# Kernel tuning notes

Measured on AMD Instinct MI355X. Metric: run time of the kernel, lower is better.

## Reference

```python
import jax, jax.numpy as jnp
import numpy as np

D_MODEL = 1024
HEADS = 16
D_K = D_MODEL // HEADS
D_FF = 4096
EPS = 1e-6


def setup_inputs() -> dict:
    key = jax.random.key(0)
    ks = jax.random.split(key, 20)
    B, S, D = 8, 1024, D_MODEL
    sc = 1.0 / np.sqrt(D)
    scf = 1.0 / np.sqrt(D_FF)
    inp = {
        "x": jax.random.normal(ks[0], (B, S, D), jnp.float32),
        "mask": jnp.ones((B, 1, 1, S), jnp.int32),
        "wq": jax.random.normal(ks[1], (D, D), jnp.float32) * sc,
        "bq": jnp.zeros((D,), jnp.float32),
        "wk": jax.random.normal(ks[2], (D, D), jnp.float32) * sc,
        "bk": jnp.zeros((D,), jnp.float32),
        "wv": jax.random.normal(ks[3], (D, D), jnp.float32) * sc,
        "bv": jnp.zeros((D,), jnp.float32),
        "wo": jax.random.normal(ks[4], (D, D), jnp.float32) * sc,
        "bo": jnp.zeros((D,), jnp.float32),
        "w1": jax.random.normal(ks[5], (D_FF, D), jnp.float32) * sc,
        "b1": jnp.zeros((D_FF,), jnp.float32),
        "w2": jax.random.normal(ks[6], (D, D_FF), jnp.float32) * scf,
        "b2": jnp.zeros((D,), jnp.float32),
        "g1": jnp.ones((D,), jnp.float32),
        "be1": jnp.zeros((D,), jnp.float32),
        "g2": jnp.ones((D,), jnp.float32),
        "be2": jnp.zeros((D,), jnp.float32),
    }
    return inp


def _layernorm(x, gamma, beta):
    # Faithful to custom LayerNorm: unbiased std (ddof=1), divide by (std+eps)
    mean = jnp.mean(x, axis=-1, keepdims=True)
    std = jnp.std(x, axis=-1, ddof=1, keepdims=True)
    return gamma * (x - mean) / (std + EPS) + beta


def _mha(x, mask, wq, bq, wk, bk, wv, bv, wo, bo):
    B, S, D = x.shape
    q = x @ wq.T + bq
    k = x @ wk.T + bk
    v = x @ wv.T + bv
    # [B,S,D] -> [B,H,S,dk]
    q = q.reshape(B, S, HEADS, D_K).transpose(0, 2, 1, 3)
    k = k.reshape(B, S, HEADS, D_K).transpose(0, 2, 1, 3)
    v = v.reshape(B, S, HEADS, D_K).transpose(0, 2, 1, 3)
    scores = jnp.einsum("bhqd,bhkd->bhqk", q, k) / np.sqrt(D_K).astype(np.float32)
    scores = jnp.where(mask == 0, jnp.float32(-1e9), scores)
    attn = jax.nn.softmax(scores, axis=-1)
    out = jnp.einsum("bhqk,bhkd->bhqd", attn, v)
    out = out.transpose(0, 2, 1, 3).reshape(B, S, D)
    return out @ wo.T + bo


def reference(x, mask, wq, bq, wk, bk, wv, bv, wo, bo, w1, b1, w2, b2, g1, be1, g2, be2):
    # residual 1: x + MHA(LN(x))
    h = _layernorm(x, g1, be1)
    x = x + _mha(h, mask, wq, bq, wk, bk, wv, bv, wo, bo)
    # residual 2: x + FFN(LN(x))
    h = _layernorm(x, g2, be2)
    ff = jax.nn.relu(h @ w1.T + b1) @ w2.T + b2
    return x + ff
```

## Files before the change

kernel.cpp:

```cpp
#include <hip/hip_runtime.h>

typedef __attribute__((ext_vector_type(8))) short short8;
typedef __attribute__((ext_vector_type(4))) short short4_t;
typedef __attribute__((ext_vector_type(4))) float floatx4;
typedef __attribute__((ext_vector_type(16))) float floatx16;

#define NTOK 8192
#define S_ 1024
#define DM 1024

__device__ __forceinline__ unsigned short f2b(float f) {
    union { float f; unsigned u; } v; v.f = f;
    unsigned r = v.u + 0x7FFF + ((v.u >> 16) & 1);
    return (unsigned short)(r >> 16);
}

__device__ __forceinline__ void gl_lds16(const void* g, void* l) {
    __builtin_amdgcn_global_load_lds((const __attribute__((address_space(1))) void*)g,
                                     (__attribute__((address_space(3))) void*)l, 16, 0, 0);
}

__global__ void cvt_f32_bf16(const float* __restrict__ src, unsigned short* __restrict__ dst, int n) {
    int i = (blockIdx.x * blockDim.x + threadIdx.x) * 4;
    if (i >= n) return;
    float4 v = *reinterpret_cast<const float4*>(src + i);
    short4_t o;
    o.x = (short)f2b(v.x); o.y = (short)f2b(v.y);
    o.z = (short)f2b(v.z); o.w = (short)f2b(v.w);
    *reinterpret_cast<short4_t*>(dst + i) = o;
}

__global__ void copy_f32(const float* __restrict__ src, float* __restrict__ dst, int n) {
    int i = (blockIdx.x * blockDim.x + threadIdx.x) * 4;
    if (i >= n) return;
    *reinterpret_cast<float4*>(dst + i) = *reinterpret_cast<const float4*>(src + i);
}

__global__ void mask_to_bias(const int* __restrict__ mask, float* __restrict__ mb, int n) {
    int i = blockIdx.x * blockDim.x + threadIdx.x;
    if (i < n) mb[i] = (mask[i] == 0) ? -1e9f : 0.f;
}

__global__ __launch_bounds__(256) void ln_kernel(const float* __restrict__ x,
                                                 const float* __restrict__ g,
                                                 const float* __restrict__ be,
                                                 unsigned short* __restrict__ out) {
    const int row = blockIdx.x;
    const int t = threadIdx.x;
    const float4 xv = *reinterpret_cast<const float4*>(x + (size_t)row * DM + t * 4);
    float s = xv.x + xv.y + xv.z + xv.w;
#pragma unroll
    for (int off = 32; off > 0; off >>= 1) s += __shfl_down(s, off);
    __shared__ float red[8];
    const int wid = t >> 6, lane = t & 63;
    if (lane == 0) red[wid] = s;
    __syncthreads();
    const float mean = (red[0] + red[1] + red[2] + red[3]) * (1.f / 1024.f);
    const float dx = xv.x - mean, dy = xv.y - mean, dz = xv.z - mean, dw = xv.w - mean;
    float ss = dx * dx + dy * dy + dz * dz + dw * dw;
#pragma unroll
    for (int off = 32; off > 0; off >>= 1) ss += __shfl_down(ss, off);
    if (lane == 0) red[4 + wid] = ss;
    __syncthreads();
    const float var = (red[4] + red[5] + red[6] + red[7]) * (1.f / 1023.f);
    const float inv = 1.f / (sqrtf(var) + 1e-6f);
    const float4 gv = *reinterpret_cast<const float4*>(g + t * 4);
    const float4 bv = *reinterpret_cast<const float4*>(be + t * 4);
    short4_t o;
    o.x = (short)f2b(gv.x * dx * inv + bv.x);
    o.y = (short)f2b(gv.y * dy * inv + bv.y);
    o.z = (short)f2b(gv.z * dz * inv + bv.z);
    o.w = (short)f2b(gv.w * dw * inv + bv.w);
    *reinterpret_cast<short4_t*>(out + (size_t)row * DM + t * 4) = o;
}

template <int EPI>
__global__ __launch_bounds__(256, 2) void gemm_bt(const unsigned short* __restrict__ A,
                                                  const unsigned short* __restrict__ Bm,
                                                  const float* __restrict__ bias,
                                                  const float* __restrict__ res,
                                                  void* __restrict__ outp,
                                                  int M, int N, int K, int tilesX) {
    __shared__ __align__(16) unsigned short lds[2][2][8192];
    const int t = threadIdx.x;
    const int lane = t & 63, wid = t >> 6;
    const int wr = wid >> 1, wc = wid & 1;

    const int nwg = gridDim.x;
    const int bid = blockIdx.x;
    const int swz = (bid & 7) * (nwg >> 3) + (bid >> 3);
    const int rowBase = (swz / tilesX) * 128;
    const int colBase = (swz % tilesX) * 128;

    const int NT = K >> 6;
    const int lr31 = lane & 31;
    const int kh = lane >> 5;

    const unsigned short* Ag[4];
    const unsigned short* Bg[4];
#pragma unroll
    for (int j = 0; j < 4; ++j) {
        const int L = j * 256 + t;
        const int r = L >> 3;
        const int c = ((L & 7) ^ (r & 7)) * 8;
        Ag[j] = A + (size_t)(rowBase + r) * K + c;
        Bg[j] = Bm + (size_t)(colBase + r) * K + c;
    }

    floatx16 acc[2][2] = {};

#pragma unroll
    for (int j = 0; j < 4; ++j) gl_lds16(Ag[j], &lds[0][0][j * 2048 + wid * 512]);
#pragma unroll
    for (int j = 0; j < 4; ++j) gl_lds16(Bg[j], &lds[0][1][j * 2048 + wid * 512]);
#pragma unroll
    for (int j = 0; j < 4; ++j) { Ag[j] += 64; Bg[j] += 64; }

    int cur = 0;
    for (int tt = 0; tt < NT; ++tt) {
        if (tt + 1 < NT) {
#pragma unroll
            for (int j = 0; j < 4; ++j)
                gl_lds16(Ag[j], &lds[cur ^ 1][0][j * 2048 + wid * 512]);
#pragma unroll
            for (int j = 0; j < 4; ++j)
                gl_lds16(Bg[j], &lds[cur ^ 1][1][j * 2048 + wid * 512]);
#pragma unroll
            for (int j = 0; j < 4; ++j) { Ag[j] += 64; Bg[j] += 64; }
            asm volatile("s_waitcnt vmcnt(8)" ::: "memory");
        } else {
            asm volatile("s_waitcnt vmcnt(0)" ::: "memory");
        }
        __builtin_amdgcn_s_barrier();
        __builtin_amdgcn_sched_barrier(0);
        const unsigned short* Ab = &lds[cur][0][0];
        const unsigned short* Bb = &lds[cur][1][0];
#pragma unroll
        for (int ks = 0; ks < 4; ++ks) {
            short8 af[2], bfr[2];
#pragma unroll
            for (int mf = 0; mf < 2; ++mf) {
                const int r = wr * 64 + mf * 32 + lr31;
                const int cp = (ks * 2 + kh) ^ (r & 7);
                af[mf] = *reinterpret_cast<const short8*>(&Ab[r * 64 + cp * 8]);
            }
#pragma unroll
            for (int nf = 0; nf < 2; ++nf) {
                const int r = wc * 64 + nf * 32 + lr31;
                const int cp = (ks * 2 + kh) ^ (r & 7);
                bfr[nf] = *reinterpret_cast<const short8*>(&Bb[r * 64 + cp * 8]);
            }
            __builtin_amdgcn_s_setprio(1);
#pragma unroll
            for (int mf = 0; mf < 2; ++mf)
#pragma unroll
                for (int nf = 0; nf < 2; ++nf)
                    acc[mf][nf] = __builtin_amdgcn_mfma_f32_32x32x16_bf16(af[mf], bfr[nf], acc[mf][nf], 0, 0, 0);
            __builtin_amdgcn_s_setprio(0);
        }
        __builtin_amdgcn_sched_barrier(0);
        __builtin_amdgcn_s_barrier();
        cur ^= 1;
    }

    const int rbw = rowBase + wr * 64;
    const int cbw = colBase + wc * 64;
    const int lc31 = lane & 31;
    if (EPI == 4) {
        unsigned short* qh = (unsigned short*)outp;
#pragma unroll
        for (int nf = 0; nf < 2; ++nf) {
            const int c = cbw + nf * 32 + lc31;
            const float bn = bias[c];
            const int sect = c >> 10;
            const int hh = (c >> 6) & 15;
            const int dd = c & 63;
#pragma unroll
            for (int mf = 0; mf < 2; ++mf) {
#pragma unroll
                for (int rg = 0; rg < 4; ++rg) {
                    const int r0 = rbw + mf * 32 + rg * 8 + 4 * kh;
                    const int bb = r0 >> 10, ss = r0 & 1023;
                    if (sect == 2) {
                        short4_t pk;
#pragma unroll
                        for (int j = 0; j < 4; ++j) pk[j] = (short)f2b(acc[mf][nf][rg * 4 + j] + bn);
                        *reinterpret_cast<short4_t*>(
                            &qh[16777216 + ((size_t)((bb * 16 + hh) * 64 + dd)) * 1024 + ss]) = pk;
                    } else {
                        unsigned short* base = qh + sect * 8388608;
#pragma unroll
                        for (int j = 0; j < 4; ++j)
                            base[((size_t)((bb * 16 + hh) * 1024 + ss + j)) * 64 + dd] =
                                f2b(acc[mf][nf][rg * 4 + j] + bn);
                    }
                }
            }
        }
        return;
    }
#pragma unroll
    for (int nf = 0; nf < 2; ++nf) {
        const int c = cbw + nf * 32 + lc31;
        const float bn = bias[c];
#pragma unroll
        for (int mf = 0; mf < 2; ++mf) {
#pragma unroll
            for (int rg = 0; rg < 4; ++rg) {
#pragma unroll
                for (int j = 0; j < 4; ++j) {
                    const int r = rbw + mf * 32 + rg * 8 + 4 * kh + j;
                    float v = acc[mf][nf][rg * 4 + j] + bn;
                    if (EPI == 1) v += res[(size_t)r * N + c];
                    if (EPI == 3) v = fmaxf(v, 0.f);
                    if (EPI == 0 || EPI == 1)
                        ((float*)outp)[(size_t)r * N + c] = v;
                    else
                        ((unsigned short*)outp)[(size_t)r * N + c] = f2b(v);
                }
            }
        }
    }
}

__global__ __launch_bounds__(256) void attn_mfma(const unsigned short* __restrict__ Qh,
                                                 const unsigned short* __restrict__ Kh,
                                                 const unsigned short* __restrict__ Vt,
                                                 const float* __restrict__ mbias,
                                                 unsigned short* __restrict__ out) {
    __shared__ __align__(16) unsigned short Kbuf[2][4096];
    __shared__ __align__(16) unsigned short Vbuf[2][4096];
    __shared__ __align__(16) unsigned short Pbuf[4][16][72];
    __shared__ __align__(16) float mk[1024];
    const int t = threadIdx.x;
    const int w = t >> 6, l = t & 63;
    const int g = l >> 4, q16 = l & 15;
    const int x7 = q16 & 7;
    const int bid = blockIdx.x;
    const int swz = (bid & 7) * 256 + (bid >> 3);
    const int bh = swz >> 4, qb = swz & 15;
    const int b = bh >> 4, h = bh & 15;

    const size_t qbase = ((size_t)bh * 1024 + qb * 64 + w * 16 + q16) * 64;
    const short8 qf0 = *reinterpret_cast<const short8*>(Qh + qbase + g * 8);
    const short8 qf1 = *reinterpret_cast<const short8*>(Qh + qbase + 32 + g * 8);

    const int r0 = t >> 3;
    const int c0 = ((t & 7) ^ (r0 & 7)) * 8;
    const unsigned short* Kg = Kh + (size_t)bh * 65536 + r0 * 64 + c0;
    const unsigned short* Vg = Vt + (size_t)bh * 65536 + r0 * 1024 + c0;

#define ATTN_STAGE(bi, kc_)                                                        \
    do {                                                                           \
        gl_lds16(Kg + (kc_) * 4096, &Kbuf[bi][w * 512]);                           \
        gl_lds16(Kg + (kc_) * 4096 + 2048, &Kbuf[bi][2048 + w * 512]);             \
        gl_lds16(Vg + (kc_) * 64, &Vbuf[bi][w * 512]);                             \
        gl_lds16(Vg + (kc_) * 64 + 32768, &Vbuf[bi][2048 + w * 512]);              \
    } while (0)

    gl_lds16(mbias + b * 1024 + t * 4, &mk[w * 256]);
    ATTN_STAGE(0, 0);

    floatx4 oacc[4] = {};
    floatx4 loacc = {};
    float m_run = -1e30f;
    const float SC2 = 0.18033688f;
    short8 ones;
#pragma unroll
    for (int j = 0; j < 8; ++j) ones[j] = (short)0x3F80;

    int cur = 0;
    for (int kc = 0; kc < 16; ++kc) {
        if (kc < 15) {
            ATTN_STAGE(cur ^ 1, kc + 1);
            asm volatile("s_waitcnt vmcnt(4)" ::: "memory");
        } else {
            asm volatile("s_waitcnt vmcnt(0)" ::: "memory");
        }
        __builtin_amdgcn_s_barrier();
        __builtin_amdgcn_sched_barrier(0);
        const unsigned short* Kb = Kbuf[cur];
        const unsigned short* Vb = Vbuf[cur];

        floatx4 st[4] = {};
        __builtin_amdgcn_s_setprio(1);
#pragma unroll
        for (int t4 = 0; t4 < 4; ++t4) {
            const int row = t4 * 16 + q16;
            const short8 kf0 = *reinterpret_cast<const short8*>(&Kb[row * 64 + (g ^ x7) * 8]);
            const short8 kf1 = *reinterpret_cast<const short8*>(&Kb[row * 64 + ((4 + g) ^ x7) * 8]);
            st[t4] = __builtin_amdgcn_mfma_f32_16x16x32_bf16(kf0, qf0, st[t4], 0, 0, 0);
            st[t4] = __builtin_amdgcn_mfma_f32_16x16x32_bf16(kf1, qf1, st[t4], 0, 0, 0);
        }
        __builtin_amdgcn_s_setprio(0);

        float mc = -1e30f;
#pragma unroll
        for (int t4 = 0; t4 < 4; ++t4) {
            const float4 mbv = *reinterpret_cast<const float4*>(&mk[kc * 64 + t4 * 16 + g * 4]);
#pragma unroll
            for (int r = 0; r < 4; ++r) {
                const float s = st[t4][r] * SC2 + ((const float*)&mbv)[r];
                st[t4][r] = s;
                mc = fmaxf(mc, s);
            }
        }
        mc = fmaxf(mc, __shfl_xor(mc, 16));
        mc = fmaxf(mc, __shfl_xor(mc, 32));
        if (__any(mc > m_run + 11.5f)) {
            const float m_new = fmaxf(m_run, mc);
            const float sc = __builtin_exp2f(m_run - m_new);
            m_run = m_new;
#pragma unroll
            for (int r = 0; r < 4; ++r) {
                const float scr = __shfl(sc, g * 4 + r);
#pragma unroll
                for (int n = 0; n < 4; ++n) oacc[n][r] *= scr;
                loacc[r] *= scr;
            }
        }
#pragma unroll
        for (int t4 = 0; t4 < 4; ++t4) {
            const float p0 = __builtin_exp2f(st[t4][0] - m_run);
            const float p1 = __builtin_exp2f(st[t4][1] - m_run);
            const float p2 = __builtin_exp2f(st[t4][2] - m_run);
            const float p3 = __builtin_exp2f(st[t4][3] - m_run);
            unsigned u0, u1;
            asm("v_cvt_pk_bf16_f32 %0, %1, %2" : "=v"(u0) : "v"(p0), "v"(p1));
            asm("v_cvt_pk_bf16_f32 %0, %1, %2" : "=v"(u1) : "v"(p2), "v"(p3));
            uint2 pr; pr.x = u0; pr.y = u1;
            *reinterpret_cast<uint2*>(&Pbuf[w][q16][t4 * 16 + g * 4]) = pr;
        }

        const short8 pf0 = *reinterpret_cast<const short8*>(&Pbuf[w][q16][g * 8]);
        const short8 pf1 = *reinterpret_cast<const short8*>(&Pbuf[w][q16][32 + g * 8]);
        __builtin_amdgcn_s_setprio(1);
        loacc = __builtin_amdgcn_mfma_f32_16x16x32_bf16(pf0, ones, loacc, 0, 0, 0);
        loacc = __builtin_amdgcn_mfma_f32_16x16x32_bf16(pf1, ones, loacc, 0, 0, 0);
#pragma unroll
        for (int n = 0; n < 4; ++n) {
            const int row = n * 16 + q16;
            const short8 vf0 = *reinterpret_cast<const short8*>(&Vb[row * 64 + (g ^ x7) * 8]);
            const short8 vf1 = *reinterpret_cast<const short8*>(&Vb[row * 64 + ((4 + g) ^ x7) * 8]);
            oacc[n] = __builtin_amdgcn_mfma_f32_16x16x32_bf16(pf0, vf0, oacc[n], 0, 0, 0);
            oacc[n] = __builtin_amdgcn_mfma_f32_16x16x32_bf16(pf1, vf1, oacc[n], 0, 0, 0);
        }
        __builtin_amdgcn_s_setprio(0);
        __builtin_amdgcn_sched_barrier(0);
        __builtin_amdgcn_s_barrier();
        cur ^= 1;
    }
#undef ATTN_STAGE

    const size_t obase = ((size_t)b * S_ + qb * 64 + w * 16) * 1024 + h * 64;
#pragma unroll
    for (int r = 0; r < 4; ++r) {
        const float invr = 1.f / loacc[r];
        const size_t orow = obase + (size_t)(g * 4 + r) * 1024;
#pragma unroll
        for (int n = 0; n < 4; ++n)
            out[orow + n * 16 + q16] = f2b(oacc[n][r] * invr);
    }
}

extern "C" void kernel_launch(void* const* d_in, const int* in_sizes, int n_in,
                              void* d_out, int out_size, void* d_ws, size_t ws_size,
                              hipStream_t stream) {
    const float* x   = (const float*)d_in[0];
    const int*  mask = (const int*)d_in[1];
    const float* wq  = (const float*)d_in[2];
    const float* bq  = (const float*)d_in[3];
    const float* wk  = (const float*)d_in[4];
    const float* bk  = (const float*)d_in[5];
    const float* wv  = (const float*)d_in[6];
    const float* bv  = (const float*)d_in[7];
    const float* wo  = (const float*)d_in[8];
    const float* bo  = (const float*)d_in[9];
    const float* w1  = (const float*)d_in[10];
    const float* b1  = (const float*)d_in[11];
    const float* w2  = (const float*)d_in[12];
    const float* b2  = (const float*)d_in[13];
    const float* g1  = (const float*)d_in[14];
    const float* be1 = (const float*)d_in[15];
    const float* g2  = (const float*)d_in[16];
    const float* be2 = (const float*)d_in[17];

    char* ws = (char*)d_ws;
    unsigned short* wqkv_bf = (unsigned short*)(ws);
    unsigned short* wo_bf   = (unsigned short*)(ws + 6291456);
    unsigned short* w1_bf   = (unsigned short*)(ws + 8388608);
    unsigned short* w2_bf   = (unsigned short*)(ws + 16777216);
    float*          bqkv    = (float*)(ws + 25165824);
    float*          mbias   = (float*)(ws + 25178112);
    unsigned short* h_bf    = (unsigned short*)(ws + 25210880);
    float*          x1      = (float*)(ws + 41988096);
    unsigned short* attn_bf = (unsigned short*)(ws + 75542528);
    unsigned short* qkvh    = (unsigned short*)(ws + 92319744);
    unsigned short* ff1_bf  = (unsigned short*)(ws + 92319744);

    cvt_f32_bf16<<<1024, 256, 0, stream>>>(wq, wqkv_bf, 1048576);
    cvt_f32_bf16<<<1024, 256, 0, stream>>>(wk, wqkv_bf + 1048576, 1048576);
    cvt_f32_bf16<<<1024, 256, 0, stream>>>(wv, wqkv_bf + 2097152, 1048576);
    cvt_f32_bf16<<<1024, 256, 0, stream>>>(wo, wo_bf, 1048576);
    cvt_f32_bf16<<<4096, 256, 0, stream>>>(w1, w1_bf, 4194304);
    cvt_f32_bf16<<<4096, 256, 0, stream>>>(w2, w2_bf, 4194304);
    copy_f32<<<1, 256, 0, stream>>>(bq, bqkv, 1024);
    copy_f32<<<1, 256, 0, stream>>>(bk, bqkv + 1024, 1024);
    copy_f32<<<1, 256, 0, stream>>>(bv, bqkv + 2048, 1024);
    mask_to_bias<<<32, 256, 0, stream>>>(mask, mbias, 8192);

    ln_kernel<<<NTOK, 256, 0, stream>>>(x, g1, be1, h_bf);
    gemm_bt<4><<<24 * 64, 256, 0, stream>>>(h_bf, wqkv_bf, bqkv, nullptr, qkvh, NTOK, 3072, 1024, 24);
    attn_mfma<<<2048, 256, 0, stream>>>(qkvh, qkvh + 8388608, qkvh + 16777216, mbias, attn_bf);
    gemm_bt<1><<<8 * 64, 256, 0, stream>>>(attn_bf, wo_bf, bo, x, x1, NTOK, 1024, 1024, 8);
    ln_kernel<<<NTOK, 256, 0, stream>>>(x1, g2, be2, h_bf);
    gemm_bt<3><<<32 * 64, 256, 0, stream>>>(h_bf, w1_bf, b1, nullptr, ff1_bf, NTOK, 4096, 1024, 32);
    gemm_bt<1><<<8 * 64, 256, 0, stream>>>(ff1_bf, w2_bf, b2, x1, (float*)d_out, NTOK, 1024, 4096, 8);
}
```

Before: 401.1 us.

## Switch GEMMs to 256x256 tiles with 512 threads and 4-stage LDS pipeline

Replaces the 128x128 double-buffered GEMM with a 256x256-tile kernel using 8 waves, each computing a 128x64 sub-tile. It uses K-steps of 32 and a 4-slot LDS ring with three loads kept in flight, a matching XOR swizzle, and a grouped 4x4 tile rasterization for L2 reuse. The larger tiles are meant to raise MFMA work per LDS read and cut global traffic. In exchange, each block needs 128KB of LDS, so only one block fits per CU, and the N=1024 GEMMs launch only 128 blocks, which may leave many CUs idle.

```diff
diff --git a/kernel.cpp b/kernel.cpp
--- a/kernel.cpp
+++ b/kernel.cpp
@@ -75,84 +75,91 @@
 }
 
 template <int EPI>
-__global__ __launch_bounds__(256, 2) void gemm_bt(const unsigned short* __restrict__ A,
+__global__ __launch_bounds__(512, 2) void gemm256(const unsigned short* __restrict__ A,
                                                   const unsigned short* __restrict__ Bm,
                                                   const float* __restrict__ bias,
                                                   const float* __restrict__ res,
                                                   void* __restrict__ outp,
                                                   int M, int N, int K, int tilesX) {
-    __shared__ __align__(16) unsigned short lds[2][2][8192];
+    __shared__ __align__(16) unsigned short lds[65536];
     const int t = threadIdx.x;
     const int lane = t & 63, wid = t >> 6;
-    const int wr = wid >> 1, wc = wid & 1;
+    const int wr = wid >> 2, wc = wid & 3;
 
     const int nwg = gridDim.x;
     const int bid = blockIdx.x;
     const int swz = (bid & 7) * (nwg >> 3) + (bid >> 3);
-    const int rowBase = (swz / tilesX) * 128;
-    const int colBase = (swz % tilesX) * 128;
-
-    const int NT = K >> 6;
+    const int bandsz = tilesX * 4;
+    const int band = swz / bandsz;
+    const int r4 = swz - band * bandsz;
+    const int sq = r4 >> 4, e = r4 & 15;
+    const int rowBase = (band * 4 + (e >> 2)) * 256;
+    const int colBase = (sq * 4 + (e & 3)) * 256;
+
+    const int NT = K >> 5;
     const int lr31 = lane & 31;
     const int kh = lane >> 5;
 
-    const unsigned short* Ag[4];
-    const unsigned short* Bg[4];
-#pragma unroll
-    for (int j = 0; j < 4; ++j) {
-        const int L = j * 256 + t;
-        const int r = L >> 3;
-        const int c = ((L & 7) ^ (r & 7)) * 8;
-        Ag[j] = A + (size_t)(rowBase + r) * K + c;
-        Bg[j] = Bm + (size_t)(colBase + r) * K + c;
-    }
-
-    floatx16 acc[2][2] = {};
-
-#pragma unroll
-    for (int j = 0; j < 4; ++j) gl_lds16(Ag[j], &lds[0][0][j * 2048 + wid * 512]);
-#pragma unroll
-    for (int j = 0; j < 4; ++j) gl_lds16(Bg[j], &lds[0][1][j * 2048 + wid * 512]);
-#pragma unroll
-    for (int j = 0; j < 4; ++j) { Ag[j] += 64; Bg[j] += 64; }
-
-    int cur = 0;
-    for (int tt = 0; tt < NT; ++tt) {
-        if (tt + 1 < NT) {
-#pragma unroll
-            for (int j = 0; j < 4; ++j)
-                gl_lds16(Ag[j], &lds[cur ^ 1][0][j * 2048 + wid * 512]);
-#pragma unroll
-            for (int j = 0; j < 4; ++j)
-                gl_lds16(Bg[j], &lds[cur ^ 1][1][j * 2048 + wid * 512]);
-#pragma unroll
-            for (int j = 0; j < 4; ++j) { Ag[j] += 64; Bg[j] += 64; }
+    const unsigned short* Asrc[2];
+    const unsigned short* Bsrc[2];
+#pragma unroll
+    for (int j = 0; j < 2; ++j) {
+        const int L = j * 512 + t;
+        const int r = L >> 2;
+        const int c = ((L & 3) ^ ((r >> 1) & 3)) * 8;
+        Asrc[j] = A + (size_t)(rowBase + r) * K + c;
+        Bsrc[j] = Bm + (size_t)(colBase + r) * K + c;
+    }
+
+#define STAGE256(kt_, s_)                                                              \
+    do {                                                                               \
+        const int _o = (kt_) * 32;                                                     \
+        gl_lds16(Asrc[0] + _o, &lds[(s_) * 16384 + wid * 512]);                        \
+        gl_lds16(Asrc[1] + _o, &lds[(s_) * 16384 + 4096 + wid * 512]);                 \
+        gl_lds16(Bsrc[0] + _o, &lds[(s_) * 16384 + 8192 + wid * 512]);                 \
+        gl_lds16(Bsrc[1] + _o, &lds[(s_) * 16384 + 12288 + wid * 512]);                \
+    } while (0)
+
+    floatx16 acc[4][2] = {};
+
+    STAGE256(0, 0);
+    STAGE256(1, 1);
+    STAGE256(2, 2);
+
+    for (int kt = 0; kt < NT; ++kt) {
+        const int slot = kt & 3;
+        if (kt + 3 < NT) {
+            STAGE256(kt + 3, (kt + 3) & 3);
+            asm volatile("s_waitcnt vmcnt(12)" ::: "memory");
+        } else if (kt + 2 < NT) {
             asm volatile("s_waitcnt vmcnt(8)" ::: "memory");
+        } else if (kt + 1 < NT) {
+            asm volatile("s_waitcnt vmcnt(4)" ::: "memory");
         } else {
             asm volatile("s_waitcnt vmcnt(0)" ::: "memory");
         }
         __builtin_amdgcn_s_barrier();
         __builtin_amdgcn_sched_barrier(0);
-        const unsigned short* Ab = &lds[cur][0][0];
-        const unsigned short* Bb = &lds[cur][1][0];
-#pragma unroll
-        for (int ks = 0; ks < 4; ++ks) {
-            short8 af[2], bfr[2];
-#pragma unroll
-            for (int mf = 0; mf < 2; ++mf) {
-                const int r = wr * 64 + mf * 32 + lr31;
-                const int cp = (ks * 2 + kh) ^ (r & 7);
-                af[mf] = *reinterpret_cast<const short8*>(&Ab[r * 64 + cp * 8]);
+        const unsigned short* Ab = &lds[slot * 16384];
+        const unsigned short* Bb = Ab + 8192;
+#pragma unroll
+        for (int ks = 0; ks < 2; ++ks) {
+            short8 af[4], bfr[2];
+#pragma unroll
+            for (int mf = 0; mf < 4; ++mf) {
+                const int r = wr * 128 + mf * 32 + lr31;
+                const int cp = (ks * 2 + kh) ^ ((r >> 1) & 3);
+                af[mf] = *reinterpret_cast<const short8*>(&Ab[r * 32 + cp * 8]);
             }
 #pragma unroll
             for (int nf = 0; nf < 2; ++nf) {
                 const int r = wc * 64 + nf * 32 + lr31;
-                const int cp = (ks * 2 + kh) ^ (r & 7);
-                bfr[nf] = *reinterpret_cast<const short8*>(&Bb[r * 64 + cp * 8]);
+                const int cp = (ks * 2 + kh) ^ ((r >> 1) & 3);
+                bfr[nf] = *reinterpret_cast<const short8*>(&Bb[r * 32 + cp * 8]);
             }
             __builtin_amdgcn_s_setprio(1);
 #pragma unroll
-            for (int mf = 0; mf < 2; ++mf)
+            for (int mf = 0; mf < 4; ++mf)
 #pragma unroll
                 for (int nf = 0; nf < 2; ++nf)
                     acc[mf][nf] = __builtin_amdgcn_mfma_f32_32x32x16_bf16(af[mf], bfr[nf], acc[mf][nf], 0, 0, 0);
@@ -160,10 +167,10 @@
         }
         __builtin_amdgcn_sched_barrier(0);
         __builtin_amdgcn_s_barrier();
-        cur ^= 1;
-    }
-
-    const int rbw = rowBase + wr * 64;
+    }
+#undef STAGE256
+
+    const int rbw = rowBase + wr * 128;
     const int cbw = colBase + wc * 64;
     const int lc31 = lane & 31;
     if (EPI == 4) {
@@ -176,7 +183,7 @@
             const int hh = (c >> 6) & 15;
             const int dd = c & 63;
 #pragma unroll
-            for (int mf = 0; mf < 2; ++mf) {
+            for (int mf = 0; mf < 4; ++mf) {
 #pragma unroll
                 for (int rg = 0; rg < 4; ++rg) {
                     const int r0 = rbw + mf * 32 + rg * 8 + 4 * kh;
@@ -204,7 +211,7 @@
         const int c = cbw + nf * 32 + lc31;
         const float bn = bias[c];
 #pragma unroll
-        for (int mf = 0; mf < 2; ++mf) {
+        for (int mf = 0; mf < 4; ++mf) {
 #pragma unroll
             for (int rg = 0; rg < 4; ++rg) {
 #pragma unroll
@@ -410,10 +417,10 @@
     mask_to_bias<<<32, 256, 0, stream>>>(mask, mbias, 8192);
 
     ln_kernel<<<NTOK, 256, 0, stream>>>(x, g1, be1, h_bf);
-    gemm_bt<4><<<24 * 64, 256, 0, stream>>>(h_bf, wqkv_bf, bqkv, nullptr, qkvh, NTOK, 3072, 1024, 24);
+    gemm256<4><<<384, 512, 0, stream>>>(h_bf, wqkv_bf, bqkv, nullptr, qkvh, NTOK, 3072, 1024, 12);
     attn_mfma<<<2048, 256, 0, stream>>>(qkvh, qkvh + 8388608, qkvh + 16777216, mbias, attn_bf);
-    gemm_bt<1><<<8 * 64, 256, 0, stream>>>(attn_bf, wo_bf, bo, x, x1, NTOK, 1024, 1024, 8);
+    gemm256<1><<<128, 512, 0, stream>>>(attn_bf, wo_bf, bo, x, x1, NTOK, 1024, 1024, 4);
     ln_kernel<<<NTOK, 256, 0, stream>>>(x1, g2, be2, h_bf);
-    gemm_bt<3><<<32 * 64, 256, 0, stream>>>(h_bf, w1_bf, b1, nullptr, ff1_bf, NTOK, 4096, 1024, 32);
-    gemm_bt<1><<<8 * 64, 256, 0, stream>>>(ff1_bf, w2_bf, b2, x1, (float*)d_out, NTOK, 1024, 4096, 8);
-}
+    gemm256<3><<<512, 512, 0, stream>>>(h_bf, w1_bf, b1, nullptr, ff1_bf, NTOK, 4096, 1024, 16);
+    gemm256<1><<<128, 512, 0, stream>>>(ff1_bf, w2_bf, b2, x1, (float*)d_out, NTOK, 1024, 4096, 4);
+}
```

Result: slower. 467.5 us (+16.6%).
